# Kernel optimization log

Measured on AMD Instinct MI355X. Metric: run time of the kernel, lower is better.

The kernel has to match this reference:

```python
import jax, jax.numpy as jnp
import numpy as np

N = 50000      # nodes per type
E = 262144     # edges per relation
D_IN = 256; D_OUT = 256; D_ATT = 64
NEG_SLOPE = 0.2


def setup_inputs() -> dict:
    key = jax.random.key(0)
    ks = jax.random.split(key, 22)
    rn = lambda k, s, sc=0.05: jax.random.normal(k, s, jnp.float32) * sc
    ri = lambda k, s: jax.random.randint(k, s, 0, N, jnp.int32)
    return {
        "hA": jax.random.normal(ks[0], (N, D_IN), jnp.float32),
        "hB": jax.random.normal(ks[1], (N, D_IN), jnp.float32),
        "Wself": rn(ks[2], (2, D_IN, D_OUT)),
        "bself": rn(ks[3], (2, D_OUT), 0.01),
        "Wq": rn(ks[4], (2, D_OUT, D_ATT)),
        "bq": rn(ks[5], (2, D_ATT), 0.01),
        "Wk": rn(ks[6], (2, D_OUT, D_ATT)),
        "bk": rn(ks[7], (2, D_ATT), 0.01),
        "Wal": rn(ks[8], (2, D_ATT)),
        "bal": rn(ks[9], (2,), 0.01),
        "War": rn(ks[10], (2, D_ATT)),
        "bar": rn(ks[11], (2,), 0.01),
        "Wsrc": rn(ks[12], (2, D_IN, D_OUT)),
        "bsrc": rn(ks[13], (2, D_OUT), 0.01),
        "Wdst": rn(ks[14], (2, D_IN, D_OUT)),
        "bdst": rn(ks[15], (2, D_OUT), 0.01),
        "attn_v": rn(ks[16], (2, D_OUT)),
        "gbias": rn(ks[17], (2, D_OUT), 0.01),
        "eab_src": ri(ks[18], (E,)),
        "eab_dst": ri(ks[19], (E,)),
        "eba_src": ri(ks[20], (E,)),
        "eba_dst": ri(ks[21], (E,)),
    }


def _gatv2(h_src, h_dst, src, dst, Ws, bs, Wd, bd, av, gb, n_dst):
    """DGL GATv2Conv, num_heads=1: e_uv = av . leaky_relu(fc_src(h)[u] + fc_dst(h)[v]),
    edge-softmax over incoming edges per dst, message = alpha * fc_src(h)[u], + bias."""
    ft_s = h_src @ Ws + bs                              # (Ns, D)
    ft_d = h_dst @ Wd + bd                              # (Nd, D)
    e = jax.nn.leaky_relu(ft_s[src] + ft_d[dst], NEG_SLOPE)  # (E, D)
    logits = e @ av                                     # (E,)
    m = jax.ops.segment_max(logits, dst, num_segments=n_dst)
    m = jnp.where(jnp.isfinite(m), m, 0.0)              # zero-in-degree safety
    ex = jnp.exp(logits - m[dst])
    den = jax.ops.segment_sum(ex, dst, num_segments=n_dst)
    alpha = ex / jnp.where(den[dst] > 0, den[dst], 1.0)  # (E,) edge softmax
    out = jax.ops.segment_sum(alpha[:, None] * ft_s[src], dst, num_segments=n_dst) + gb
    return out, alpha


def _forward(hA, hB, Wself, bself, Wq, bq, Wk, bk, Wal, bal, War, bar,
             Wsrc, bsrc, Wdst, bdst, attn_v, gbias,
             eab_src, eab_dst, eba_src, eba_dst):
    h = [hA, hB]
    z = [h[t] @ Wself[t] + bself[t] for t in range(2)]       # HeteroLinear W_self
    q = [z[t] @ Wq[t] + bq[t] for t in range(2)]
    k = [z[t] @ Wk[t] + bk[t] for t in range(2)]
    h_l = [k[t] @ Wal[t] + bal[t] for t in range(2)]          # (N,) = W_al(key)
    h_r = [q[t] @ War[t] + bar[t] for t in range(2)]          # (N,) = W_ar(query)
    att_self = [jax.nn.elu(h_l[t] + h_r[t]) for t in range(2)]

    # relation "ab": A -> B (etype index 0)
    rst_ab, a_ab = _gatv2(hA, hB, eab_src, eab_dst,
                          Wsrc[0], bsrc[0], Wdst[0], bdst[0], attn_v[0], gbias[0], N)
    eatt_b = jax.nn.elu((rst_ab @ Wk[1] + bk[1]) @ Wal[1] + bal[1] + h_r[1])
    # relation "ba": B -> A (etype index 1)
    rst_ba, a_ba = _gatv2(hB, hA, eba_src, eba_dst,
                          Wsrc[1], bsrc[1], Wdst[1], bdst[1], attn_v[1], gbias[1], N)
    eatt_a = jax.nn.elu((rst_ba @ Wk[0] + bk[0]) @ Wal[0] + bal[0] + h_r[0])

    attA = jax.nn.softmax(jnp.stack([att_self[0], eatt_a]), axis=0)  # (2, N)
    attB = jax.nn.softmax(jnp.stack([att_self[1], eatt_b]), axis=0)
    rstA = jax.nn.elu(attA[0][:, None] * z[0] + attA[1][:, None] * rst_ba)
    rstB = jax.nn.elu(attB[0][:, None] * z[1] + attB[1][:, None] * rst_ab)
    return jnp.stack([rstA, rstB])  # (2, N, D_OUT)


def reference(hA, hB, Wself, bself, Wq, bq, Wk, bk, Wal, bal, War, bar,
              Wsrc, bsrc, Wdst, bdst, attn_v, gbias,
              eab_src, eab_dst, eba_src, eba_dst):
    return _forward(hA, hB, Wself, bself, Wq, bq, Wk, bk, Wal, bal, War, bar,
                    Wsrc, bsrc, Wdst, bdst, attn_v, gbias,
                    eab_src, eab_dst, eba_src, eba_dst)
```

## Files before the change

### kernel.cpp

```cpp
#include <hip/hip_runtime.h>
#include <math.h>

#define NNODES 50000
#define NEDGES 262144
#define NEG_SLOPE 0.2f
#define NBINS (2 * NNODES)
#define NXP 391
#define NWG_GEMM (2 * NXP * 6)

typedef __attribute__((ext_vector_type(8))) short short8;
typedef __attribute__((ext_vector_type(8))) unsigned short u16x8;
typedef __attribute__((ext_vector_type(4))) float f32x4;
typedef __attribute__((ext_vector_type(4))) unsigned short u16x4;

__device__ __forceinline__ float elu_f(float x) { return x > 0.f ? x : (__expf(x) - 1.f); }
__device__ __forceinline__ float bf2f(unsigned short u) {
    return __uint_as_float(((unsigned)u) << 16);
}
__device__ __forceinline__ unsigned short f2bf(float f) {
    unsigned u = __float_as_uint(f);
    unsigned r = (u + 0x7fffu + ((u >> 16) & 1u)) >> 16;
    return (unsigned short)r;
}

__global__ __launch_bounds__(256) void conv_bf16_2(const float* __restrict__ inA,
                                                   const float* __restrict__ inB,
                                                   unsigned short* __restrict__ outA,
                                                   unsigned short* __restrict__ outB,
                                                   int half) {
    int i = (blockIdx.x * 256 + threadIdx.x) * 4;
    if (i >= 2 * half) return;
    const float* in = (i < half) ? inA : inB;
    unsigned short* out = (i < half) ? outA : outB;
    int k = (i < half) ? i : i - half;
    float4 v = *reinterpret_cast<const float4*>(&in[k]);
    u16x4 o;
    o[0] = f2bf(v.x); o[1] = f2bf(v.y); o[2] = f2bf(v.z); o[3] = f2bf(v.w);
    *reinterpret_cast<u16x4*>(&out[k]) = o;
}

__global__ __launch_bounds__(256) void prep_w(
    const float* __restrict__ Wself, const float* __restrict__ Wsrc, const float* __restrict__ Wdst,
    const float* __restrict__ bself, const float* __restrict__ bsrc, const float* __restrict__ bdst,
    unsigned short* __restrict__ Wt, float* __restrict__ biasF) {
    int r = blockIdx.x;
    int t = r / 768;
    int n = r % 768;
    int seg = n >> 8;
    int nn = n & 255;
    const float* W; const float* bv; int ti;
    if (seg == 0)      { W = Wself; bv = bself; ti = t; }
    else if (seg == 1) { W = Wsrc;  bv = bsrc;  ti = t; }
    else               { W = Wdst;  bv = bdst;  ti = 1 - t; }
    int k = threadIdx.x;
    float val = W[(size_t)ti * 65536 + (size_t)k * 256 + nn];
    Wt[(size_t)r * 256 + k] = f2bf(val);
    if (k == 0) biasF[r] = bv[ti * 256 + nn];
}

__global__ __launch_bounds__(256) void precompute_uv(
    const float* __restrict__ Wq, const float* __restrict__ bq,
    const float* __restrict__ Wk, const float* __restrict__ bk,
    const float* __restrict__ Wal, const float* __restrict__ bal,
    const float* __restrict__ War, const float* __restrict__ bar,
    float* __restrict__ u_l, float* __restrict__ u_r,
    float* __restrict__ c_l, float* __restrict__ c_r) {
    int t = blockIdx.x;
    int d = threadIdx.x;
    float sl = 0.f, sr = 0.f;
    for (int j = 0; j < 64; ++j) {
        sl += Wk[((size_t)t * 256 + d) * 64 + j] * Wal[t * 64 + j];
        sr += Wq[((size_t)t * 256 + d) * 64 + j] * War[t * 64 + j];
    }
    u_l[t * 256 + d] = sl;
    u_r[t * 256 + d] = sr;
    if (d == 0) {
        float cl = bal[t], cr = bar[t];
        for (int j = 0; j < 64; ++j) {
            cl += bk[t * 64 + j] * Wal[t * 64 + j];
            cr += bq[t * 64 + j] * War[t * 64 + j];
        }
        c_l[t] = cl; c_r[t] = cr;
    }
}

__global__ __launch_bounds__(256) void hist2(const int* __restrict__ dab,
                                             const int* __restrict__ dba,
                                             int* __restrict__ counts) {
    int e = blockIdx.x * 256 + threadIdx.x;
    if (e < NEDGES) atomicAdd(&counts[dab[e]], 1);
    else if (e < 2 * NEDGES) atomicAdd(&counts[NNODES + dba[e - NEDGES]], 1);
}

__global__ __launch_bounds__(256) void scan1(const int* __restrict__ counts,
                                             int* __restrict__ incl,
                                             int* __restrict__ bsum, int n) {
    __shared__ int s[256];
    int i = blockIdx.x * 256 + threadIdx.x;
    int t = threadIdx.x;
    s[t] = (i < n) ? counts[i] : 0;
    __syncthreads();
#pragma unroll
    for (int off = 1; off < 256; off <<= 1) {
        int x = (t >= off) ? s[t - off] : 0;
        __syncthreads();
        s[t] += x;
        __syncthreads();
    }
    if (i < n) incl[i] = s[t];
    if (t == 255) bsum[blockIdx.x] = s[255];
}

__global__ __launch_bounds__(512) void scan2(int* __restrict__ bsum, int nb) {
    __shared__ int s[512];
    int t = threadIdx.x;
    s[t] = (t < nb) ? bsum[t] : 0;
    __syncthreads();
#pragma unroll
    for (int off = 1; off < 512; off <<= 1) {
        int x = (t >= off) ? s[t - off] : 0;
        __syncthreads();
        s[t] += x;
        __syncthreads();
    }
    if (t < nb) bsum[t] = s[t];
}

__global__ __launch_bounds__(256) void scan3(const int* __restrict__ counts,
                                             int* __restrict__ incl_to_excl,
                                             const int* __restrict__ bsum,
                                             int* __restrict__ cursor, int n) {
    int i = blockIdx.x * 256 + threadIdx.x;
    if (i >= n) return;
    int base = (blockIdx.x > 0) ? bsum[blockIdx.x - 1] : 0;
    int st = base + incl_to_excl[i] - counts[i];
    incl_to_excl[i] = st;
    cursor[i] = st;
}

__global__ __launch_bounds__(256) void scatter2(const int* __restrict__ sab,
                                                const int* __restrict__ dab,
                                                const int* __restrict__ sba,
                                                const int* __restrict__ dba,
                                                int* __restrict__ cursor,
                                                int* __restrict__ sorted_src) {
    int e = blockIdx.x * 256 + threadIdx.x;
    if (e < NEDGES) {
        int pos = atomicAdd(&cursor[dab[e]], 1);
        sorted_src[pos] = sab[e];
    } else if (e < 2 * NEDGES) {
        int k = e - NEDGES;
        int pos = atomicAdd(&cursor[NNODES + dba[k]], 1);
        sorted_src[pos] = sba[k];
    }
}

__global__ __launch_bounds__(256) void gemm_mfma(
    const unsigned short* __restrict__ hAb,
    const unsigned short* __restrict__ hBb,
    const unsigned short* __restrict__ Wt,
    const float* __restrict__ biasF,
    unsigned short* __restrict__ bufA,
    unsigned short* __restrict__ bufB,
    int M)
{
    __shared__ unsigned short lds[16384];
    const int tid = threadIdx.x;
    const int lane = tid & 63;
    const int w = tid >> 6;
    const int wm = w >> 1, wn = w & 1;

    const int nwg = NWG_GEMM;
    const int q = nwg / 8, r = nwg % 8;
    int orig = blockIdx.x;
    int xcd = orig % 8, idx = orig / 8;
    int wgid = (xcd < r) ? (xcd * (q + 1) + idx) : (r * (q + 1) + (xcd - r) * q + idx);
    int t   = wgid / (NXP * 6);
    int rem = wgid % (NXP * 6);
    int xp  = rem / 6;
    int yc  = rem % 6;

    const int row0 = xp * 128;
    const int col0 = yc * 128;
    const unsigned short* Ain = t ? hBb : hAb;
    const unsigned short* Wtt = Wt + (size_t)t * 768 * 256;
    const float* bias = biasF + t * 768;
    unsigned short* Cout = t ? bufB : bufA;

    f32x4 acc[4][4] = {};

    const unsigned short* gA[2];
    const unsigned short* gB[2];
#pragma unroll
    for (int rr = 0; rr < 2; ++rr) {
        int qq = rr * 256 + tid;
        int row = qq >> 2;
        int c = (qq & 3) ^ ((row >> 1) & 3);
        int ga = min(row0 + row, M - 1);
        gA[rr] = Ain + (size_t)ga * 256 + c * 8;
        gB[rr] = Wtt + (size_t)(col0 + row) * 256 + c * 8;
    }

#define STAGE(buf, kt)                                                                   \
    {                                                                                    \
        unsigned short* Ad = lds + (buf) * 4096;                                         \
        unsigned short* Bd = lds + 8192 + (buf) * 4096;                                  \
        _Pragma("unroll")                                                                \
        for (int rr = 0; rr < 2; ++rr) {                                                 \
            __builtin_amdgcn_global_load_lds(                                            \
                (const __attribute__((address_space(1))) unsigned int*)(gA[rr] + (kt)),  \
                (__attribute__((address_space(3))) unsigned int*)(Ad + ((rr * 256 + w * 64) << 3)), \
                16, 0, 0);                                                               \
            __builtin_amdgcn_global_load_lds(                                            \
                (const __attribute__((address_space(1))) unsigned int*)(gB[rr] + (kt)),  \
                (__attribute__((address_space(3))) unsigned int*)(Bd + ((rr * 256 + w * 64) << 3)), \
                16, 0, 0);                                                               \
        }                                                                                \
    }

    STAGE(0, 0);
    __syncthreads();

#pragma unroll
    for (int it = 0; it < 8; ++it) {
        const int cur = it & 1;
        if (it < 7) STAGE(cur ^ 1, (it + 1) * 32);
        const unsigned short* As = lds + cur * 4096;
        const unsigned short* Bs = lds + 8192 + cur * 4096;
        short8 a[4], b[4];
#pragma unroll
        for (int i = 0; i < 4; ++i) {
            int ar = wm * 64 + i * 16 + (lane & 15);
            a[i] = *reinterpret_cast<const short8*>(
                &As[ar * 32 + (((lane >> 4) ^ ((ar >> 1) & 3)) << 3)]);
            int br = wn * 64 + i * 16 + (lane & 15);
            b[i] = *reinterpret_cast<const short8*>(
                &Bs[br * 32 + (((lane >> 4) ^ ((br >> 1) & 3)) << 3)]);
        }
#pragma unroll
        for (int i = 0; i < 4; ++i)
#pragma unroll
            for (int j = 0; j < 4; ++j)
                acc[i][j] = __builtin_amdgcn_mfma_f32_16x16x32_bf16(a[i], b[j], acc[i][j], 0, 0, 0);
        __syncthreads();
    }
#undef STAGE

#pragma unroll
    for (int j = 0; j < 4; ++j) {
        int colg = wn * 4 + j;
        int ci = lane & 15;
        float bv = bias[col0 + colg * 16 + ci];
#pragma unroll
        for (int i = 0; i < 4; ++i) {
            int rowb = wm * 64 + i * 16 + ((lane >> 4) << 2);
#pragma unroll
            for (int v = 0; v < 4; ++v) {
                int row = rowb + v;
                int g2 = colg ^ ((row >> 2) & 3);
                lds[row * 128 + g2 * 16 + ci] = f2bf(acc[i][j][v] + bv);
            }
        }
    }
    __syncthreads();
#pragma unroll
    for (int p = 0; p < 8; ++p) {
        int idx = p * 256 + tid;
        int row = idx >> 4;
        int ch = idx & 15;
        int g2 = (ch >> 1) ^ ((row >> 2) & 3);
        int grow = row0 + row;
        if (grow < M)
            *reinterpret_cast<short8*>(&Cout[(size_t)grow * 768 + col0 + ch * 8]) =
                *reinterpret_cast<const short8*>(&lds[row * 128 + g2 * 16 + ((ch & 1) << 3)]);
    }
}

__global__ __launch_bounds__(256) void gat_fused(
    const unsigned short* __restrict__ bufA, const unsigned short* __restrict__ bufB,
    const int* __restrict__ sorted_src, const int* __restrict__ row_start,
    const int* __restrict__ counts,
    const float* __restrict__ attn_v, const float* __restrict__ gbias,
    const float* __restrict__ u_l, const float* __restrict__ u_r,
    const float* __restrict__ c_l, const float* __restrict__ c_r,
    float* __restrict__ out)
{
    const int tid = threadIdx.x;
    const int l = tid & 15;
    const int gBase = tid & 48;
    const int nd = blockIdx.x * 16 + (tid >> 4);
    if (nd >= 2 * NNODES) return;
    const int rel = nd >= NNODES;
    const int d = nd - rel * NNODES;
    const int td = rel ? 0 : 1;

    const unsigned short* zbuf = td ? bufB : bufA;
    const unsigned short* ftS = (rel ? bufB : bufA) + 256;
    const unsigned short* ftD = zbuf + 512;
    const float* av = attn_v + (rel ? 256 : 0);
    const float* gb = gbias  + (rel ? 256 : 0);
    const float* ul = u_l + td * 256;
    const float* ur = u_r + td * 256;
    const float clv = c_l[td], crv = c_r[td];
    const unsigned short* zrow = zbuf + (size_t)d * 768;

    float fd[16], avv[16], ulv[16];
    {
        u16x8 d0 = *reinterpret_cast<const u16x8*>(&ftD[(size_t)d * 768 + l * 16]);
        u16x8 d1 = *reinterpret_cast<const u16x8*>(&ftD[(size_t)d * 768 + l * 16 + 8]);
#pragma unroll
        for (int e = 0; e < 8; ++e) { fd[e] = bf2f(d0[e]); fd[8 + e] = bf2f(d1[e]); }
#pragma unroll
        for (int e = 0; e < 4; ++e) {
            float4 a = *reinterpret_cast<const float4*>(&av[l * 16 + e * 4]);
            avv[4*e] = a.x; avv[4*e+1] = a.y; avv[4*e+2] = a.z; avv[4*e+3] = a.w;
            float4 u = *reinterpret_cast<const float4*>(&ul[l * 16 + e * 4]);
            ulv[4*e] = u.x; ulv[4*e+1] = u.y; ulv[4*e+2] = u.z; ulv[4*e+3] = u.w;
        }
    }

    float hl = 0.f, hr = 0.f;
    {
        u16x8 z0 = *reinterpret_cast<const u16x8*>(&zrow[l * 16]);
        u16x8 z1 = *reinterpret_cast<const u16x8*>(&zrow[l * 16 + 8]);
#pragma unroll
        for (int e = 0; e < 4; ++e) {
            float4 u = *reinterpret_cast<const float4*>(&ur[l * 16 + e * 4]);
            float zf0 = bf2f(z0[2*e]), zf1 = bf2f(z0[2*e+1]);
            (void)u; (void)zf0; (void)zf1;
        }
        float zf[16];
#pragma unroll
        for (int e = 0; e < 8; ++e) { zf[e] = bf2f(z0[e]); zf[8 + e] = bf2f(z1[e]); }
#pragma unroll
        for (int e = 0; e < 4; ++e) {
            float4 u = *reinterpret_cast<const float4*>(&ur[l * 16 + e * 4]);
            hr += zf[4*e] * u.x + zf[4*e+1] * u.y + zf[4*e+2] * u.z + zf[4*e+3] * u.w;
        }
#pragma unroll
        for (int e = 0; e < 16; ++e) hl += zf[e] * ulv[e];
    }
    hl += __shfl_xor(hl, 1); hr += __shfl_xor(hr, 1);
    hl += __shfl_xor(hl, 2); hr += __shfl_xor(hr, 2);
    hl += __shfl_xor(hl, 4); hr += __shfl_xor(hr, 4);
    hl += __shfl_xor(hl, 8); hr += __shfl_xor(hr, 8);
    hl += clv; hr += crv;
    const float a0 = elu_f(hl + hr);

    const int p0  = row_start[nd];
    const int cnt = counts[nd];
    float den = 0.f;
    float acc[16] = {};

    for (int base = 0; base < cnt; base += 16) {
        int nloc = min(16, cnt - base);
        int sv = (base + l < cnt) ? sorted_src[p0 + base + l] : 0;
        int j = 0;
        for (; j + 2 <= nloc; j += 2) {
            int s0 = __shfl(sv, gBase + j);
            int s1 = __shfl(sv, gBase + j + 1);
            const unsigned short* rp0 = &ftS[(size_t)s0 * 768 + l * 16];
            const unsigned short* rp1 = &ftS[(size_t)s1 * 768 + l * 16];
            u16x8 a0v = *reinterpret_cast<const u16x8*>(rp0);
            u16x8 a1v = *reinterpret_cast<const u16x8*>(rp0 + 8);
            u16x8 b0v = *reinterpret_cast<const u16x8*>(rp1);
            u16x8 b1v = *reinterpret_cast<const u16x8*>(rp1 + 8);
            float fa[16], fb[16];
            float pa = 0.f, pb = 0.f;
#pragma unroll
            for (int e = 0; e < 8; ++e) {
                fa[e] = bf2f(a0v[e]);  fa[8 + e] = bf2f(a1v[e]);
                fb[e] = bf2f(b0v[e]);  fb[8 + e] = bf2f(b1v[e]);
            }
#pragma unroll
            for (int e = 0; e < 16; ++e) {
                float xa = fa[e] + fd[e];
                pa += avv[e] * fmaxf(xa, NEG_SLOPE * xa);
                float xb = fb[e] + fd[e];
                pb += avv[e] * fmaxf(xb, NEG_SLOPE * xb);
            }
            pa += __shfl_xor(pa, 1); pb += __shfl_xor(pb, 1);
            pa += __shfl_xor(pa, 2); pb += __shfl_xor(pb, 2);
            pa += __shfl_xor(pa, 4); pb += __shfl_xor(pb, 4);
            pa += __shfl_xor(pa, 8); pb += __shfl_xor(pb, 8);
            float wa = __expf(pa), wb = __expf(pb);
            den += wa + wb;
#pragma unroll
            for (int e = 0; e < 16; ++e) acc[e] += wa * fa[e] + wb * fb[e];
        }
        if (j < nloc) {
            int s0 = __shfl(sv, gBase + j);
            const unsigned short* rp0 = &ftS[(size_t)s0 * 768 + l * 16];
            u16x8 a0v = *reinterpret_cast<const u16x8*>(rp0);
            u16x8 a1v = *reinterpret_cast<const u16x8*>(rp0 + 8);
            float fa[16];
            float pa = 0.f;
#pragma unroll
            for (int e = 0; e < 8; ++e) { fa[e] = bf2f(a0v[e]); fa[8 + e] = bf2f(a1v[e]); }
#pragma unroll
            for (int e = 0; e < 16; ++e) {
                float xa = fa[e] + fd[e];
                pa += avv[e] * fmaxf(xa, NEG_SLOPE * xa);
            }
            pa += __shfl_xor(pa, 1);
            pa += __shfl_xor(pa, 2);
            pa += __shfl_xor(pa, 4);
            pa += __shfl_xor(pa, 8);
            float wa = __expf(pa);
            den += wa;
#pragma unroll
            for (int e = 0; e < 16; ++e) acc[e] += wa * fa[e];
        }
    }

    float inv = den > 0.f ? 1.f / den : 1.f;
    float v[16];
#pragma unroll
    for (int e = 0; e < 4; ++e) {
        float4 g = *reinterpret_cast<const float4*>(&gb[l * 16 + e * 4]);
        v[4*e]   = acc[4*e]   * inv + g.x;
        v[4*e+1] = acc[4*e+1] * inv + g.y;
        v[4*e+2] = acc[4*e+2] * inv + g.z;
        v[4*e+3] = acc[4*e+3] * inv + g.w;
    }

    float dotv = 0.f;
#pragma unroll
    for (int e = 0; e < 16; ++e) dotv += v[e] * ulv[e];
    dotv += __shfl_xor(dotv, 1);
    dotv += __shfl_xor(dotv, 2);
    dotv += __shfl_xor(dotv, 4);
    dotv += __shfl_xor(dotv, 8);
    const float ea = elu_f(dotv + clv + hr);

    float mx = fmaxf(a0, ea);
    float e0 = __expf(a0 - mx), e1 = __expf(ea - mx);
    float is = 1.f / (e0 + e1);
    float w0 = e0 * is, w1 = e1 * is;

    u16x8 z0 = *reinterpret_cast<const u16x8*>(&zrow[l * 16]);
    u16x8 z1 = *reinterpret_cast<const u16x8*>(&zrow[l * 16 + 8]);
    float zf[16];
#pragma unroll
    for (int e = 0; e < 8; ++e) { zf[e] = bf2f(z0[e]); zf[8 + e] = bf2f(z1[e]); }

    float* orow = out + ((size_t)(1 - rel) * NNODES + d) * 256 + l * 16;
#pragma unroll
    for (int e = 0; e < 4; ++e) {
        float4 o;
        o.x = elu_f(w0 * zf[4*e]   + w1 * v[4*e]);
        o.y = elu_f(w0 * zf[4*e+1] + w1 * v[4*e+1]);
        o.z = elu_f(w0 * zf[4*e+2] + w1 * v[4*e+2]);
        o.w = elu_f(w0 * zf[4*e+3] + w1 * v[4*e+3]);
        *reinterpret_cast<float4*>(&orow[e * 4]) = o;
    }
}

extern "C" void kernel_launch(void* const* d_in, const int* in_sizes, int n_in,
                              void* d_out, int out_size, void* d_ws, size_t ws_size,
                              hipStream_t stream) {
    const float* hA     = (const float*)d_in[0];
    const float* hB     = (const float*)d_in[1];
    const float* Wself  = (const float*)d_in[2];
    const float* bself  = (const float*)d_in[3];
    const float* Wq     = (const float*)d_in[4];
    const float* bq     = (const float*)d_in[5];
    const float* Wk     = (const float*)d_in[6];
    const float* bk     = (const float*)d_in[7];
    const float* Wal    = (const float*)d_in[8];
    const float* bal    = (const float*)d_in[9];
    const float* War    = (const float*)d_in[10];
    const float* bar    = (const float*)d_in[11];
    const float* Wsrc   = (const float*)d_in[12];
    const float* bsrc   = (const float*)d_in[13];
    const float* Wdst   = (const float*)d_in[14];
    const float* bdst   = (const float*)d_in[15];
    const float* attn_v = (const float*)d_in[16];
    const float* gbias  = (const float*)d_in[17];
    const int* eab_src  = (const int*)d_in[18];
    const int* eab_dst  = (const int*)d_in[19];
    const int* eba_src  = (const int*)d_in[20];
    const int* eba_dst  = (const int*)d_in[21];
    float* out = (float*)d_out;
    char* ws = (char*)d_ws;

    const size_t SZ_BUF = (size_t)NNODES * 768 * sizeof(unsigned short);
    const size_t SZ_H   = (size_t)NNODES * 256 * sizeof(unsigned short);
    size_t off = 0;
    auto alloc = [&](size_t bytes) { void* p = ws + off; off = (off + bytes + 255) & ~(size_t)255; return p; };
    unsigned short* bufA = (unsigned short*)alloc(SZ_BUF);
    unsigned short* bufB = (unsigned short*)alloc(SZ_BUF);
    unsigned short* hAb  = (unsigned short*)alloc(SZ_H);
    unsigned short* hBb  = (unsigned short*)alloc(SZ_H);
    unsigned short* Wt   = (unsigned short*)alloc(2 * 768 * 256 * sizeof(unsigned short));
    float* biasF   = (float*)alloc(2 * 768 * sizeof(float));
    int* counts    = (int*)alloc(NBINS * sizeof(int));
    int* row_start = (int*)alloc(NBINS * sizeof(int));
    int* cursor    = (int*)alloc(NBINS * sizeof(int));
    int* bsum      = (int*)alloc(512 * sizeof(int));
    int* sorted_src= (int*)alloc(2 * (size_t)NEDGES * sizeof(int));
    float* u_l     = (float*)alloc(2 * 256 * sizeof(float));
    float* u_r     = (float*)alloc(2 * 256 * sizeof(float));
    float* c_l     = (float*)alloc(2 * sizeof(float));
    float* c_r     = (float*)alloc(2 * sizeof(float));

    hipMemsetAsync(counts, 0, NBINS * sizeof(int), stream);
    precompute_uv<<<2, 256, 0, stream>>>(Wq, bq, Wk, bk, Wal, bal, War, bar, u_l, u_r, c_l, c_r);

    const int HN = NNODES * 256;
    conv_bf16_2<<<(2 * HN / 4 + 255) / 256, 256, 0, stream>>>(hA, hB, hAb, hBb, HN);
    prep_w<<<2 * 768, 256, 0, stream>>>(Wself, Wsrc, Wdst, bself, bsrc, bdst, Wt, biasF);

    const int e2blocks = (2 * NEDGES + 255) / 256;
    hist2<<<e2blocks, 256, 0, stream>>>(eab_dst, eba_dst, counts);
    const int sblocks = (NBINS + 255) / 256;
    scan1<<<sblocks, 256, 0, stream>>>(counts, row_start, bsum, NBINS);
    scan2<<<1, 512, 0, stream>>>(bsum, sblocks);
    scan3<<<sblocks, 256, 0, stream>>>(counts, row_start, bsum, cursor, NBINS);
    scatter2<<<e2blocks, 256, 0, stream>>>(eab_src, eab_dst, eba_src, eba_dst, cursor, sorted_src);

    gemm_mfma<<<NWG_GEMM, 256, 0, stream>>>(hAb, hBb, Wt, biasF, bufA, bufB, NNODES);

    gat_fused<<<(2 * NNODES + 15) / 16, 256, 0, stream>>>(bufA, bufB, sorted_src, row_start,
                                                          counts, attn_v, gbias,
                                                          u_l, u_r, c_l, c_r, out);
}
```

Baseline: 270.6 us.

## Decompose leaky-relu logit into per-node dots computed in GEMM epilogue

Rewrites leaky_relu(x) as 0.6x + 0.4|x|. The linear part of each edge logit then splits into per-node dot products with attn_v. The GEMM epilogue now computes these, plus the hl/hr projections, and accumulates them into an aux buffer with atomics. The edge loop only evaluates the |x| term, and the gather kernel no longer recomputes the z-row dot products. The GEMM main loop also switches to a deeper prefetch schedule with explicit vmcnt waits and barriers. This adds atomics, an extra memset and fp32 reordering changes in exchange for less per-edge work.

```diff
diff --git a/kernel.cpp b/kernel.cpp
--- a/kernel.cpp
+++ b/kernel.cpp
@@ -9,13 +9,24 @@
 #define NWG_GEMM (2 * NXP * 6)
 
 typedef __attribute__((ext_vector_type(8))) short short8;
-typedef __attribute__((ext_vector_type(8))) unsigned short u16x8;
 typedef __attribute__((ext_vector_type(4))) float f32x4;
+typedef __attribute__((ext_vector_type(2))) float f32x2;
 typedef __attribute__((ext_vector_type(4))) unsigned short u16x4;
+
+#define AUX_PS 0
+#define AUX_PD (2 * NNODES)
+#define AUX_HL (4 * NNODES)
+#define AUX_HR (6 * NNODES)
 
 __device__ __forceinline__ float elu_f(float x) { return x > 0.f ? x : (__expf(x) - 1.f); }
 __device__ __forceinline__ float bf2f(unsigned short u) {
     return __uint_as_float(((unsigned)u) << 16);
+}
+__device__ __forceinline__ f32x2 bfp2f(unsigned p) {
+    f32x2 r;
+    r.x = __uint_as_float(p << 16);
+    r.y = __uint_as_float(p & 0xffff0000u);
+    return r;
 }
 __device__ __forceinline__ unsigned short f2bf(float f) {
     unsigned u = __float_as_uint(f);
@@ -160,8 +171,12 @@
     const unsigned short* __restrict__ hBb,
     const unsigned short* __restrict__ Wt,
     const float* __restrict__ biasF,
+    const float* __restrict__ attn_v,
+    const float* __restrict__ u_l,
+    const float* __restrict__ u_r,
     unsigned short* __restrict__ bufA,
     unsigned short* __restrict__ bufB,
+    float* __restrict__ aux,
     int M)
 {
     __shared__ unsigned short lds[16384];
@@ -219,12 +234,16 @@
     }
 
     STAGE(0, 0);
-    __syncthreads();
+    STAGE(1, 32);
 
 #pragma unroll
     for (int it = 0; it < 8; ++it) {
         const int cur = it & 1;
-        if (it < 7) STAGE(cur ^ 1, (it + 1) * 32);
+        if (it < 7) { asm volatile("s_waitcnt vmcnt(4)" ::: "memory"); }
+        else        { asm volatile("s_waitcnt vmcnt(0)" ::: "memory"); }
+        __builtin_amdgcn_s_barrier();
+        __builtin_amdgcn_sched_barrier(0);
+
         const unsigned short* As = lds + cur * 4096;
         const unsigned short* Bs = lds + 8192 + cur * 4096;
         short8 a[4], b[4];
@@ -242,7 +261,11 @@
 #pragma unroll
             for (int j = 0; j < 4; ++j)
                 acc[i][j] = __builtin_amdgcn_mfma_f32_16x16x32_bf16(a[i], b[j], acc[i][j], 0, 0, 0);
-        __syncthreads();
+
+        asm volatile("s_waitcnt lgkmcnt(0)" ::: "memory");
+        __builtin_amdgcn_sched_barrier(0);
+        __builtin_amdgcn_s_barrier();
+        if (it < 6) STAGE(cur, (it + 2) * 32);
     }
 #undef STAGE
 
@@ -263,6 +286,19 @@
         }
     }
     __syncthreads();
+
+    const int seg = yc >> 1;
+    const float* avp1; float* axp1;
+    const float* avp2 = nullptr; float* axp2 = nullptr;
+    if (seg == 0) {
+        avp1 = u_l + t * 256;            axp1 = aux + AUX_HL + (size_t)t * NNODES;
+        avp2 = u_r + t * 256;            axp2 = aux + AUX_HR + (size_t)t * NNODES;
+    } else if (seg == 1) {
+        avp1 = attn_v + t * 256;         axp1 = aux + AUX_PS + (size_t)t * NNODES;
+    } else {
+        avp1 = attn_v + (1 - t) * 256;   axp1 = aux + AUX_PD + (size_t)(1 - t) * NNODES;
+    }
+
 #pragma unroll
     for (int p = 0; p < 8; ++p) {
         int idx = p * 256 + tid;
@@ -270,9 +306,35 @@
         int ch = idx & 15;
         int g2 = (ch >> 1) ^ ((row >> 2) & 3);
         int grow = row0 + row;
-        if (grow < M)
-            *reinterpret_cast<short8*>(&Cout[(size_t)grow * 768 + col0 + ch * 8]) =
-                *reinterpret_cast<const short8*>(&lds[row * 128 + g2 * 16 + ((ch & 1) << 3)]);
+        bool ok = grow < M;
+        short8 val = *reinterpret_cast<const short8*>(&lds[row * 128 + g2 * 16 + ((ch & 1) << 3)]);
+        if (ok)
+            *reinterpret_cast<short8*>(&Cout[(size_t)grow * 768 + col0 + ch * 8]) = val;
+        int colb = (yc & 1) * 128 + ch * 8;
+        float4 w0v = *reinterpret_cast<const float4*>(&avp1[colb]);
+        float4 w1v = *reinterpret_cast<const float4*>(&avp1[colb + 4]);
+        float p1 = w0v.x * bf2f((unsigned short)val[0]) + w0v.y * bf2f((unsigned short)val[1])
+                 + w0v.z * bf2f((unsigned short)val[2]) + w0v.w * bf2f((unsigned short)val[3])
+                 + w1v.x * bf2f((unsigned short)val[4]) + w1v.y * bf2f((unsigned short)val[5])
+                 + w1v.z * bf2f((unsigned short)val[6]) + w1v.w * bf2f((unsigned short)val[7]);
+        p1 += __shfl_xor(p1, 1);
+        p1 += __shfl_xor(p1, 2);
+        p1 += __shfl_xor(p1, 4);
+        p1 += __shfl_xor(p1, 8);
+        if ((tid & 15) == 0 && ok) atomicAdd(&axp1[grow], p1);
+        if (avp2) {
+            float4 y0 = *reinterpret_cast<const float4*>(&avp2[colb]);
+            float4 y1 = *reinterpret_cast<const float4*>(&avp2[colb + 4]);
+            float p2 = y0.x * bf2f((unsigned short)val[0]) + y0.y * bf2f((unsigned short)val[1])
+                     + y0.z * bf2f((unsigned short)val[2]) + y0.w * bf2f((unsigned short)val[3])
+                     + y1.x * bf2f((unsigned short)val[4]) + y1.y * bf2f((unsigned short)val[5])
+                     + y1.z * bf2f((unsigned short)val[6]) + y1.w * bf2f((unsigned short)val[7]);
+            p2 += __shfl_xor(p2, 1);
+            p2 += __shfl_xor(p2, 2);
+            p2 += __shfl_xor(p2, 4);
+            p2 += __shfl_xor(p2, 8);
+            if ((tid & 15) == 0 && ok) atomicAdd(&axp2[grow], p2);
+        }
     }
 }
 
@@ -281,8 +343,9 @@
     const int* __restrict__ sorted_src, const int* __restrict__ row_start,
     const int* __restrict__ counts,
     const float* __restrict__ attn_v, const float* __restrict__ gbias,
-    const float* __restrict__ u_l, const float* __restrict__ u_r,
+    const float* __restrict__ u_l,
     const float* __restrict__ c_l, const float* __restrict__ c_r,
+    const float* __restrict__ aux,
     float* __restrict__ out)
 {
     const int tid = threadIdx.x;
@@ -297,161 +360,147 @@
     const unsigned short* zbuf = td ? bufB : bufA;
     const unsigned short* ftS = (rel ? bufB : bufA) + 256;
     const unsigned short* ftD = zbuf + 512;
-    const float* av = attn_v + (rel ? 256 : 0);
-    const float* gb = gbias  + (rel ? 256 : 0);
-    const float* ul = u_l + td * 256;
-    const float* ur = u_r + td * 256;
     const float clv = c_l[td], crv = c_r[td];
-    const unsigned short* zrow = zbuf + (size_t)d * 768;
-
-    float fd[16], avv[16], ulv[16];
+
+    f32x2 fd2[8], av2[8];
     {
-        u16x8 d0 = *reinterpret_cast<const u16x8*>(&ftD[(size_t)d * 768 + l * 16]);
-        u16x8 d1 = *reinterpret_cast<const u16x8*>(&ftD[(size_t)d * 768 + l * 16 + 8]);
-#pragma unroll
-        for (int e = 0; e < 8; ++e) { fd[e] = bf2f(d0[e]); fd[8 + e] = bf2f(d1[e]); }
+        const unsigned short* fdp = &ftD[(size_t)d * 768 + l * 16];
+        uint4 d0 = *reinterpret_cast<const uint4*>(fdp);
+        uint4 d1 = *reinterpret_cast<const uint4*>(fdp + 8);
+        fd2[0] = bfp2f(d0.x); fd2[1] = bfp2f(d0.y); fd2[2] = bfp2f(d0.z); fd2[3] = bfp2f(d0.w);
+        fd2[4] = bfp2f(d1.x); fd2[5] = bfp2f(d1.y); fd2[6] = bfp2f(d1.z); fd2[7] = bfp2f(d1.w);
+        const float* avp = attn_v + rel * 256 + l * 16;
 #pragma unroll
         for (int e = 0; e < 4; ++e) {
-            float4 a = *reinterpret_cast<const float4*>(&av[l * 16 + e * 4]);
-            avv[4*e] = a.x; avv[4*e+1] = a.y; avv[4*e+2] = a.z; avv[4*e+3] = a.w;
-            float4 u = *reinterpret_cast<const float4*>(&ul[l * 16 + e * 4]);
-            ulv[4*e] = u.x; ulv[4*e+1] = u.y; ulv[4*e+2] = u.z; ulv[4*e+3] = u.w;
-        }
-    }
-
-    float hl = 0.f, hr = 0.f;
-    {
-        u16x8 z0 = *reinterpret_cast<const u16x8*>(&zrow[l * 16]);
-        u16x8 z1 = *reinterpret_cast<const u16x8*>(&zrow[l * 16 + 8]);
-#pragma unroll
-        for (int e = 0; e < 4; ++e) {
-            float4 u = *reinterpret_cast<const float4*>(&ur[l * 16 + e * 4]);
-            float zf0 = bf2f(z0[2*e]), zf1 = bf2f(z0[2*e+1]);
-            (void)u; (void)zf0; (void)zf1;
-        }
-        float zf[16];
-#pragma unroll
-        for (int e = 0; e < 8; ++e) { zf[e] = bf2f(z0[e]); zf[8 + e] = bf2f(z1[e]); }
-#pragma unroll
-        for (int e = 0; e < 4; ++e) {
-            float4 u = *reinterpret_cast<const float4*>(&ur[l * 16 + e * 4]);
-            hr += zf[4*e] * u.x + zf[4*e+1] * u.y + zf[4*e+2] * u.z + zf[4*e+3] * u.w;
-        }
-#pragma unroll
-        for (int e = 0; e < 16; ++e) hl += zf[e] * ulv[e];
-    }
-    hl += __shfl_xor(hl, 1); hr += __shfl_xor(hr, 1);
-    hl += __shfl_xor(hl, 2); hr += __shfl_xor(hr, 2);
-    hl += __shfl_xor(hl, 4); hr += __shfl_xor(hr, 4);
-    hl += __shfl_xor(hl, 8); hr += __shfl_xor(hr, 8);
-    hl += clv; hr += crv;
-    const float a0 = elu_f(hl + hr);
+            float4 a = *reinterpret_cast<const float4*>(&avp[e * 4]);
+            av2[2 * e].x = a.x; av2[2 * e].y = a.y;
+            av2[2 * e + 1].x = a.z; av2[2 * e + 1].y = a.w;
+        }
+    }
+
+    const float pd6 = 0.6f * aux[AUX_PD + (size_t)rel * NNODES + d];
+    const float hlv = aux[AUX_HL + (size_t)td * NNODES + d] + clv;
+    const float hrv = aux[AUX_HR + (size_t)td * NNODES + d] + crv;
+    const float a0 = elu_f(hlv + hrv);
+    const float* psb = aux + AUX_PS + (size_t)rel * NNODES;
 
     const int p0  = row_start[nd];
     const int cnt = counts[nd];
     float den = 0.f;
-    float acc[16] = {};
+    f32x2 acc2[8];
+#pragma unroll
+    for (int e = 0; e < 8; ++e) { acc2[e].x = 0.f; acc2[e].y = 0.f; }
 
     for (int base = 0; base < cnt; base += 16) {
         int nloc = min(16, cnt - base);
-        int sv = (base + l < cnt) ? sorted_src[p0 + base + l] : 0;
+        int sv = 0; float psl = 0.f;
+        if (base + l < cnt) { sv = sorted_src[p0 + base + l]; psl = psb[sv]; }
         int j = 0;
         for (; j + 2 <= nloc; j += 2) {
             int s0 = __shfl(sv, gBase + j);
             int s1 = __shfl(sv, gBase + j + 1);
+            float q0 = __shfl(psl, gBase + j);
+            float q1 = __shfl(psl, gBase + j + 1);
             const unsigned short* rp0 = &ftS[(size_t)s0 * 768 + l * 16];
             const unsigned short* rp1 = &ftS[(size_t)s1 * 768 + l * 16];
-            u16x8 a0v = *reinterpret_cast<const u16x8*>(rp0);
-            u16x8 a1v = *reinterpret_cast<const u16x8*>(rp0 + 8);
-            u16x8 b0v = *reinterpret_cast<const u16x8*>(rp1);
-            u16x8 b1v = *reinterpret_cast<const u16x8*>(rp1 + 8);
-            float fa[16], fb[16];
-            float pa = 0.f, pb = 0.f;
+            uint4 A0 = *reinterpret_cast<const uint4*>(rp0);
+            uint4 A1 = *reinterpret_cast<const uint4*>(rp0 + 8);
+            uint4 B0 = *reinterpret_cast<const uint4*>(rp1);
+            uint4 B1 = *reinterpret_cast<const uint4*>(rp1 + 8);
+            f32x2 fa2[8], fb2[8];
+            fa2[0] = bfp2f(A0.x); fa2[1] = bfp2f(A0.y); fa2[2] = bfp2f(A0.z); fa2[3] = bfp2f(A0.w);
+            fa2[4] = bfp2f(A1.x); fa2[5] = bfp2f(A1.y); fa2[6] = bfp2f(A1.z); fa2[7] = bfp2f(A1.w);
+            fb2[0] = bfp2f(B0.x); fb2[1] = bfp2f(B0.y); fb2[2] = bfp2f(B0.z); fb2[3] = bfp2f(B0.w);
+            fb2[4] = bfp2f(B1.x); fb2[5] = bfp2f(B1.y); fb2[6] = bfp2f(B1.z); fb2[7] = bfp2f(B1.w);
+            float Sa = 0.f, Sb = 0.f;
 #pragma unroll
             for (int e = 0; e < 8; ++e) {
-                fa[e] = bf2f(a0v[e]);  fa[8 + e] = bf2f(a1v[e]);
-                fb[e] = bf2f(b0v[e]);  fb[8 + e] = bf2f(b1v[e]);
+                f32x2 xa = fa2[e] + fd2[e];
+                f32x2 xb = fb2[e] + fd2[e];
+                Sa += av2[e].x * fabsf(xa.x);
+                Sa += av2[e].y * fabsf(xa.y);
+                Sb += av2[e].x * fabsf(xb.x);
+                Sb += av2[e].y * fabsf(xb.y);
             }
-#pragma unroll
-            for (int e = 0; e < 16; ++e) {
-                float xa = fa[e] + fd[e];
-                pa += avv[e] * fmaxf(xa, NEG_SLOPE * xa);
-                float xb = fb[e] + fd[e];
-                pb += avv[e] * fmaxf(xb, NEG_SLOPE * xb);
-            }
-            pa += __shfl_xor(pa, 1); pb += __shfl_xor(pb, 1);
-            pa += __shfl_xor(pa, 2); pb += __shfl_xor(pb, 2);
-            pa += __shfl_xor(pa, 4); pb += __shfl_xor(pb, 4);
-            pa += __shfl_xor(pa, 8); pb += __shfl_xor(pb, 8);
-            float wa = __expf(pa), wb = __expf(pb);
+            Sa += __shfl_xor(Sa, 1); Sb += __shfl_xor(Sb, 1);
+            Sa += __shfl_xor(Sa, 2); Sb += __shfl_xor(Sb, 2);
+            Sa += __shfl_xor(Sa, 4); Sb += __shfl_xor(Sb, 4);
+            Sa += __shfl_xor(Sa, 8); Sb += __shfl_xor(Sb, 8);
+            float wa = __expf(fmaf(0.6f, q0, pd6) + 0.4f * Sa);
+            float wb = __expf(fmaf(0.6f, q1, pd6) + 0.4f * Sb);
             den += wa + wb;
 #pragma unroll
-            for (int e = 0; e < 16; ++e) acc[e] += wa * fa[e] + wb * fb[e];
+            for (int e = 0; e < 8; ++e) acc2[e] += wa * fa2[e] + wb * fb2[e];
         }
         if (j < nloc) {
             int s0 = __shfl(sv, gBase + j);
+            float q0 = __shfl(psl, gBase + j);
             const unsigned short* rp0 = &ftS[(size_t)s0 * 768 + l * 16];
-            u16x8 a0v = *reinterpret_cast<const u16x8*>(rp0);
-            u16x8 a1v = *reinterpret_cast<const u16x8*>(rp0 + 8);
-            float fa[16];
-            float pa = 0.f;
-#pragma unroll
-            for (int e = 0; e < 8; ++e) { fa[e] = bf2f(a0v[e]); fa[8 + e] = bf2f(a1v[e]); }
-#pragma unroll
-            for (int e = 0; e < 16; ++e) {
-                float xa = fa[e] + fd[e];
-                pa += avv[e] * fmaxf(xa, NEG_SLOPE * xa);
+            uint4 A0 = *reinterpret_cast<const uint4*>(rp0);
+            uint4 A1 = *reinterpret_cast<const uint4*>(rp0 + 8);
+            f32x2 fa2[8];
+            fa2[0] = bfp2f(A0.x); fa2[1] = bfp2f(A0.y); fa2[2] = bfp2f(A0.z); fa2[3] = bfp2f(A0.w);
+            fa2[4] = bfp2f(A1.x); fa2[5] = bfp2f(A1.y); fa2[6] = bfp2f(A1.z); fa2[7] = bfp2f(A1.w);
+            float Sa = 0.f;
+#pragma unroll
+            for (int e = 0; e < 8; ++e) {
+                f32x2 xa = fa2[e] + fd2[e];
+                Sa += av2[e].x * fabsf(xa.x);
+                Sa += av2[e].y * fabsf(xa.y);
             }
-            pa += __shfl_xor(pa, 1);
-            pa += __shfl_xor(pa, 2);
-            pa += __shfl_xor(pa, 4);
-            pa += __shfl_xor(pa, 8);
-            float wa = __expf(pa);
+            Sa += __shfl_xor(Sa, 1);
+            Sa += __shfl_xor(Sa, 2);
+            Sa += __shfl_xor(Sa, 4);
+            Sa += __shfl_xor(Sa, 8);
+            float wa = __expf(fmaf(0.6f, q0, pd6) + 0.4f * Sa);
             den += wa;
 #pragma unroll
-            for (int e = 0; e < 16; ++e) acc[e] += wa * fa[e];
+            for (int e = 0; e < 8; ++e) acc2[e] += wa * fa2[e];
         }
     }
 
     float inv = den > 0.f ? 1.f / den : 1.f;
-    float v[16];
+    const float* gb = gbias + rel * 256 + l * 16;
+    const float* ulp = u_l + td * 256 + l * 16;
+    f32x2 v2[8];
+    float dotv = 0.f;
 #pragma unroll
     for (int e = 0; e < 4; ++e) {
-        float4 g = *reinterpret_cast<const float4*>(&gb[l * 16 + e * 4]);
-        v[4*e]   = acc[4*e]   * inv + g.x;
-        v[4*e+1] = acc[4*e+1] * inv + g.y;
-        v[4*e+2] = acc[4*e+2] * inv + g.z;
-        v[4*e+3] = acc[4*e+3] * inv + g.w;
-    }
-
-    float dotv = 0.f;
-#pragma unroll
-    for (int e = 0; e < 16; ++e) dotv += v[e] * ulv[e];
+        float4 g = *reinterpret_cast<const float4*>(&gb[e * 4]);
+        float4 u = *reinterpret_cast<const float4*>(&ulp[e * 4]);
+        v2[2 * e].x     = acc2[2 * e].x     * inv + g.x;
+        v2[2 * e].y     = acc2[2 * e].y     * inv + g.y;
+        v2[2 * e + 1].x = acc2[2 * e + 1].x * inv + g.z;
+        v2[2 * e + 1].y = acc2[2 * e + 1].y * inv + g.w;
+        dotv += v2[2 * e].x * u.x + v2[2 * e].y * u.y
+              + v2[2 * e + 1].x * u.z + v2[2 * e + 1].y * u.w;
+    }
     dotv += __shfl_xor(dotv, 1);
     dotv += __shfl_xor(dotv, 2);
     dotv += __shfl_xor(dotv, 4);
     dotv += __shfl_xor(dotv, 8);
-    const float ea = elu_f(dotv + clv + hr);
+    const float ea = elu_f(dotv + clv + hrv);
 
     float mx = fmaxf(a0, ea);
     float e0 = __expf(a0 - mx), e1 = __expf(ea - mx);
     float is = 1.f / (e0 + e1);
     float w0 = e0 * is, w1 = e1 * is;
 
-    u16x8 z0 = *reinterpret_cast<const u16x8*>(&zrow[l * 16]);
-    u16x8 z1 = *reinterpret_cast<const u16x8*>(&zrow[l * 16 + 8]);
-    float zf[16];
-#pragma unroll
-    for (int e = 0; e < 8; ++e) { zf[e] = bf2f(z0[e]); zf[8 + e] = bf2f(z1[e]); }
+    const unsigned short* zrow = zbuf + (size_t)d * 768 + l * 16;
+    uint4 z0 = *reinterpret_cast<const uint4*>(zrow);
+    uint4 z1 = *reinterpret_cast<const uint4*>(zrow + 8);
+    f32x2 zf2[8];
+    zf2[0] = bfp2f(z0.x); zf2[1] = bfp2f(z0.y); zf2[2] = bfp2f(z0.z); zf2[3] = bfp2f(z0.w);
+    zf2[4] = bfp2f(z1.x); zf2[5] = bfp2f(z1.y); zf2[6] = bfp2f(z1.z); zf2[7] = bfp2f(z1.w);
 
     float* orow = out + ((size_t)(1 - rel) * NNODES + d) * 256 + l * 16;
 #pragma unroll
     for (int e = 0; e < 4; ++e) {
         float4 o;
-        o.x = elu_f(w0 * zf[4*e]   + w1 * v[4*e]);
-        o.y = elu_f(w0 * zf[4*e+1] + w1 * v[4*e+1]);
-        o.z = elu_f(w0 * zf[4*e+2] + w1 * v[4*e+2]);
-        o.w = elu_f(w0 * zf[4*e+3] + w1 * v[4*e+3]);
+        o.x = elu_f(w0 * zf2[2 * e].x     + w1 * v2[2 * e].x);
+        o.y = elu_f(w0 * zf2[2 * e].y     + w1 * v2[2 * e].y);
+        o.z = elu_f(w0 * zf2[2 * e + 1].x + w1 * v2[2 * e + 1].x);
+        o.w = elu_f(w0 * zf2[2 * e + 1].y + w1 * v2[2 * e + 1].y);
         *reinterpret_cast<float4*>(&orow[e * 4]) = o;
     }
 }
@@ -494,6 +543,7 @@
     unsigned short* hBb  = (unsigned short*)alloc(SZ_H);
     unsigned short* Wt   = (unsigned short*)alloc(2 * 768 * 256 * sizeof(unsigned short));
     float* biasF   = (float*)alloc(2 * 768 * sizeof(float));
+    float* aux     = (float*)alloc((size_t)8 * NNODES * sizeof(float));
     int* counts    = (int*)alloc(NBINS * sizeof(int));
     int* row_start = (int*)alloc(NBINS * sizeof(int));
     int* cursor    = (int*)alloc(NBINS * sizeof(int));
@@ -505,6 +555,7 @@
     float* c_r     = (float*)alloc(2 * sizeof(float));
 
     hipMemsetAsync(counts, 0, NBINS * sizeof(int), stream);
+    hipMemsetAsync(aux, 0, (size_t)8 * NNODES * sizeof(float), stream);
     precompute_uv<<<2, 256, 0, stream>>>(Wq, bq, Wk, bk, Wal, bal, War, bar, u_l, u_r, c_l, c_r);
 
     const int HN = NNODES * 256;
@@ -519,9 +570,10 @@
     scan3<<<sblocks, 256, 0, stream>>>(counts, row_start, bsum, cursor, NBINS);
     scatter2<<<e2blocks, 256, 0, stream>>>(eab_src, eab_dst, eba_src, eba_dst, cursor, sorted_src);
 
-    gemm_mfma<<<NWG_GEMM, 256, 0, stream>>>(hAb, hBb, Wt, biasF, bufA, bufB, NNODES);
+    gemm_mfma<<<NWG_GEMM, 256, 0, stream>>>(hAb, hBb, Wt, biasF, attn_v, u_l, u_r,
+                                            bufA, bufB, aux, NNODES);
 
     gat_fused<<<(2 * NNODES + 15) / 16, 256, 0, stream>>>(bufA, bufB, sorted_src, row_start,
-                                                          counts, attn_v, gbias,
-                                                          u_l, u_r, c_l, c_r, out);
-}
+                                                          counts, attn_v, gbias, u_l,
+                                                          c_l, c_r, aux, out);
+}
```

New measurement: 272.6 us. No clear change (+0.8%).
